# Optimization experiments

Hardware: AMD Instinct MI355X
Metric: run time of the kernel (lower is better)

Reference implementation:

```python
import jax, jax.numpy as jnp
import numpy as np

RADIUS = 1.0      # cfg['radius']
NEAR = 0.5        # cfg['near']
N_STEPS = 32      # cfg['ray_marching_steps']
N_SECANT = 8      # n_secant_steps in unisurf()
TAU = 0.5         # occupancy decision threshold
EPS = 1e-6        # module-level epsilon


def _occ(p, W1, b1, W2, b2):
    # stand-in occupancy network: [..., 3] -> [...]
    h = jax.nn.relu(p @ W1 + b1)
    return jax.nn.sigmoid(h @ W2 + b2)[..., 0]


def get_sphere_intersection(cam_loc, rays, r=RADIUS):
    # cam_loc: [B,3], rays: [B,P,3] (unit). Faithful to the torch version.
    ray_cam_dot = jnp.einsum('bpd,bd->bp', rays, cam_loc)                    # [B,P]
    under_sqrt = ray_cam_dot ** 2 - (jnp.sum(cam_loc ** 2, -1, keepdims=True) - r * r)
    mask_intersect = under_sqrt > 0
    s = jnp.sqrt(jnp.where(mask_intersect, under_sqrt, 0.0))
    inter = jnp.stack([-s - ray_cam_dot, s - ray_cam_dot], axis=-1)          # [B,P,2]
    inter = jnp.where(mask_intersect[..., None], inter, 0.0)
    return jnp.maximum(inter, 0.0), mask_intersect


def setup_inputs() -> dict:
    key = jax.random.key(0)
    k1, k2, k3, k4, k5, k6 = jax.random.split(key, 6)
    B, P, H = 1, 131072, 32
    # camera ~2 units from origin; rays aimed at points near the unit sphere
    cam_loc = jnp.array([[0.0, 0.0, 2.0]], dtype=jnp.float32) + 0.01 * jax.random.normal(k1, (B, 3))
    targets = 0.3 * jax.random.normal(k2, (B, P, 3))
    ray_directions = (targets - cam_loc[:, None, :]).astype(jnp.float32)
    W1 = (0.8 * jax.random.normal(k3, (3, H))).astype(jnp.float32)
    b1 = (0.1 * jax.random.normal(k4, (H,))).astype(jnp.float32)
    W2 = (0.5 * jax.random.normal(k5, (H, 1))).astype(jnp.float32)
    b2 = (0.1 * jax.random.normal(k6, (1,))).astype(jnp.float32)
    return {"cam_loc": cam_loc, "ray_directions": ray_directions,
            "W1": W1, "b1": b1, "W2": W2, "b2": b2}


def reference(cam_loc, ray_directions, W1, b1, W2, b2):
    rays = ray_directions / jnp.linalg.norm(ray_directions, axis=-1, keepdims=True)
    inter, mask_int = get_sphere_intersection(cam_loc, rays, RADIUS)
    far = jnp.maximum(inter[..., 1], NEAR + EPS)                             # [B,P]

    # coarse march: N_STEPS samples per ray between near and sphere-far
    t = jnp.linspace(0.0, 1.0, N_STEPS, dtype=jnp.float32)                   # [S]
    d = NEAR * (1.0 - t) + far[..., None] * t                                # [B,P,S]
    p = cam_loc[:, None, None, :] + rays[:, :, None, :] * d[..., None]       # [B,P,S,3]
    f = _occ(p, W1, b1, W2, b2) - TAU                                        # [B,P,S]

    # first free->occupied sign change (masked-index pattern, vectorized)
    cross = (f[..., :-1] < 0) & (f[..., 1:] >= 0)                            # [B,P,S-1]
    found = jnp.any(cross, axis=-1) & mask_int                               # [B,P]
    idx = jnp.argmax(cross, axis=-1)                                         # [B,P]

    def take(a, i):
        return jnp.take_along_axis(a, i[..., None], axis=-1)[..., 0]

    d_low, f_low = take(d, idx), take(f, idx)
    d_high, f_high = take(d, idx + 1), take(f, idx + 1)

    def secant_body(_, c):
        dl, fl, dh, fh = c
        den = fh - fl
        den = jnp.where(jnp.abs(den) < EPS, EPS, den)
        dm = dl - fl * (dh - dl) / den
        pm = cam_loc[:, None, :] + rays * dm[..., None]
        fm = _occ(pm, W1, b1, W2, b2) - TAU
        neg = fm < 0
        return (jnp.where(neg, dm, dl), jnp.where(neg, fm, fl),
                jnp.where(neg, dh, dm), jnp.where(neg, fh, fm))

    d_low, f_low, d_high, f_high = jax.lax.fori_loop(
        0, N_SECANT, secant_body, (d_low, f_low, d_high, f_high))
    den = f_high - f_low
    den = jnp.where(jnp.abs(den) < EPS, EPS, den)
    d_mid = d_low - f_low * (d_high - d_low) / den
    d_pred = jnp.where(found, d_mid, 0.0)                                    # [B,P]

    # surface points fed back to the model (depth detached, as in torch)
    p_surf = cam_loc[:, None, :] + rays * jax.lax.stop_gradient(d_pred)[..., None]
    occ_surf = jnp.where(found, _occ(p_surf, W1, b1, W2, b2), 0.0)           # [B,P]
    return d_pred, occ_surf
```

## Files before the change

### kernel.cpp

```cpp
#include <hip/hip_runtime.h>
#include <math.h>

#define HDIM 32
#define NSTEPS 32
#define NSECANT 8
#define RADIUSV 1.0f
#define NEARV 0.5f
#define TAUV 0.5f
#define EPSV 1e-6f

typedef float f2 __attribute__((ext_vector_type(2)));

__global__ __launch_bounds__(256) void unisurf_kernel(
    const float* __restrict__ cam_loc,
    const float* __restrict__ ray_dirs,
    const float* __restrict__ W1,
    const float* __restrict__ b1,
    const float* __restrict__ W2,
    const float* __restrict__ b2,
    float* __restrict__ out,
    int P)
{
    __shared__ float4 sW[HDIM];
    __shared__ float  sW2[HDIM];
    __shared__ float  sB2;

    const int tid = threadIdx.x;
    if (tid < HDIM) {
        sW[tid] = make_float4(W1[tid], W1[HDIM + tid], W1[2 * HDIM + tid], b1[tid]);
        sW2[tid] = W2[tid];
    }
    if (tid == 0) sB2 = b2[0];
    __syncthreads();

    const int i = blockIdx.x * blockDim.x + tid;
    if (i >= P) return;

    const float cx = cam_loc[0], cy = cam_loc[1], cz = cam_loc[2];

    float dx = ray_dirs[3 * i + 0];
    float dy = ray_dirs[3 * i + 1];
    float dz = ray_dirs[3 * i + 2];
    float nrm = sqrtf(dx * dx + dy * dy + dz * dz);
    float rx = dx / nrm, ry = dy / nrm, rz = dz / nrm;

    float rcd = rx * cx + ry * cy + rz * cz;
    float c2  = cx * cx + cy * cy + cz * cz;
    float us  = rcd * rcd - (c2 - RADIUSV * RADIUSV);
    bool  mask_int = us > 0.0f;
    float s_sq = mask_int ? sqrtf(us) : 0.0f;
    float far_raw = mask_int ? fmaxf(s_sq - rcd, 0.0f) : 0.0f;
    float farv = fmaxf(far_raw, NEARV + EPSV);

    f2 rW[HDIM / 2], cW[HDIM / 2], w2[HDIM / 2];
    #pragma unroll
    for (int h = 0; h < HDIM / 2; ++h) {
        float4 wa = sW[2 * h], wb = sW[2 * h + 1];
        rW[h] = (f2){rx * wa.x + ry * wa.y + rz * wa.z,
                     rx * wb.x + ry * wb.y + rz * wb.z};
        cW[h] = (f2){cx * wa.x + cy * wa.y + cz * wa.z + wa.w,
                     cx * wb.x + cy * wb.y + cz * wb.z + wb.w};
        w2[h] = (f2){sW2[2 * h], sW2[2 * h + 1]};
    }
    const float B2 = sB2;
    const f2 z2 = (f2){0.0f, 0.0f};

    auto logit = [&](float d) -> float {
        f2 dv = (f2){d, d};
        f2 a0 = z2, a1 = z2, a2 = z2, a3 = z2;
        #pragma unroll
        for (int h = 0; h < HDIM / 2; h += 4) {
            f2 x0 = __builtin_elementwise_fma(dv, rW[h + 0], cW[h + 0]);
            f2 x1 = __builtin_elementwise_fma(dv, rW[h + 1], cW[h + 1]);
            f2 x2 = __builtin_elementwise_fma(dv, rW[h + 2], cW[h + 2]);
            f2 x3 = __builtin_elementwise_fma(dv, rW[h + 3], cW[h + 3]);
            a0 = __builtin_elementwise_fma(__builtin_elementwise_max(x0, z2), w2[h + 0], a0);
            a1 = __builtin_elementwise_fma(__builtin_elementwise_max(x1, z2), w2[h + 1], a1);
            a2 = __builtin_elementwise_fma(__builtin_elementwise_max(x2, z2), w2[h + 2], a2);
            a3 = __builtin_elementwise_fma(__builtin_elementwise_max(x3, z2), w2[h + 3], a3);
        }
        f2 aa = (a0 + a1) + (a2 + a3);
        return (aa.x + aa.y) + B2;
    };
    auto sigm = [](float x) -> float {
        float e = __expf(-x);
        return __builtin_amdgcn_rcpf(1.0f + e);
    };

    float l_prev = logit(NEARV);
    float d_prev = NEARV;
    const float l0 = l_prev;
    float d1v = 0.0f, l1v = 0.0f;

    bool found = false;
    float d_lo = 0.0f, l_lo = 0.0f, d_hi = 0.0f, l_hi = 0.0f;

    const float STEPC = 0.03225806451612903f;
    #pragma unroll 2
    for (int s = 1; s < NSTEPS; ++s) {
        float t = (float)s * STEPC;
        float dd = NEARV * (1.0f - t) + farv * t;
        float ls = logit(dd);
        if (s == 1) { d1v = dd; l1v = ls; }
        if (!found && (l_prev < 0.0f) && (ls >= 0.0f)) {
            found = true;
            d_lo = d_prev; l_lo = l_prev;
            d_hi = dd;     l_hi = ls;
        }
        d_prev = dd; l_prev = ls;
    }
    if (!found) {
        d_lo = NEARV; l_lo = l0;
        d_hi = d1v;   l_hi = l1v;
    }
    found = found && mask_int;

    float f_lo = sigm(l_lo) - TAUV;
    float f_hi = sigm(l_hi) - TAUV;

    #pragma unroll 1
    for (int it = 0; it < NSECANT; ++it) {
        float den = f_hi - f_lo;
        den = (fabsf(den) < EPSV) ? EPSV : den;
        float dm = d_lo - f_lo * (d_hi - d_lo) * __builtin_amdgcn_rcpf(den);
        float fm = sigm(logit(dm)) - TAUV;
        bool neg = fm < 0.0f;
        d_lo = neg ? dm : d_lo;
        f_lo = neg ? fm : f_lo;
        d_hi = neg ? d_hi : dm;
        f_hi = neg ? f_hi : fm;
    }
    float den = f_hi - f_lo;
    den = (fabsf(den) < EPSV) ? EPSV : den;
    float d_mid = d_lo - f_lo * (d_hi - d_lo) * __builtin_amdgcn_rcpf(den);

    float d_pred = found ? d_mid : 0.0f;
    float occ_s = sigm(logit(d_pred));
    float occ_surf = found ? occ_s : 0.0f;

    out[i]     = d_pred;
    out[P + i] = occ_surf;
}

extern "C" void kernel_launch(void* const* d_in, const int* in_sizes, int n_in,
                              void* d_out, int out_size, void* d_ws, size_t ws_size,
                              hipStream_t stream) {
    const float* cam_loc  = (const float*)d_in[0];
    const float* ray_dirs = (const float*)d_in[1];
    const float* W1       = (const float*)d_in[2];
    const float* b1       = (const float*)d_in[3];
    const float* W2       = (const float*)d_in[4];
    const float* b2       = (const float*)d_in[5];
    float* out = (float*)d_out;

    const int P = in_sizes[1] / 3;
    const int block = 256;
    const int grid = (P + block - 1) / block;
    unisurf_kernel<<<grid, block, 0, stream>>>(cam_loc, ray_dirs, W1, b1, W2, b2, out, P);
}
```

Measured before the change: 21.04 us.

## Split each ray's MLP across two lanes and combine with ds_swizzle

Each ray is now handled by a pair of adjacent threads. Each thread evaluates half of the 32 hidden units, and the partial logits are summed through a ds_swizzle pair exchange, so both lanes follow the same marching and secant control flow. This doubles the thread count and halves per-thread registers and FMA work, aiming to raise occupancy and hide latency on a grid that was otherwise small. The cost is duplicated scalar work per ray (normalization, loop control, secant updates) and an extra cross-lane exchange on every network evaluation.

Measured after the change: 22.65 us. 1.08x slower.

```diff
diff --git a/kernel.cpp b/kernel.cpp
--- a/kernel.cpp
+++ b/kernel.cpp
@@ -10,6 +10,11 @@
 #define EPSV 1e-6f
 
 typedef float f2 __attribute__((ext_vector_type(2)));
+
+__device__ __forceinline__ float pair_other(float x) {
+    return __builtin_bit_cast(float,
+        __builtin_amdgcn_ds_swizzle(__builtin_bit_cast(int, x), 0x041F));
+}
 
 __global__ __launch_bounds__(256) void unisurf_kernel(
     const float* __restrict__ cam_loc,
@@ -33,14 +38,17 @@
     if (tid == 0) sB2 = b2[0];
     __syncthreads();
 
-    const int i = blockIdx.x * blockDim.x + tid;
-    if (i >= P) return;
+    const int j = blockIdx.x * blockDim.x + tid;
+    const int r = j >> 1;
+    if (r >= P) return;
+    const int sub = j & 1;
+    const int ubase = sub * (HDIM / 2);
 
     const float cx = cam_loc[0], cy = cam_loc[1], cz = cam_loc[2];
 
-    float dx = ray_dirs[3 * i + 0];
-    float dy = ray_dirs[3 * i + 1];
-    float dz = ray_dirs[3 * i + 2];
+    float dx = ray_dirs[3 * r + 0];
+    float dy = ray_dirs[3 * r + 1];
+    float dz = ray_dirs[3 * r + 2];
     float nrm = sqrtf(dx * dx + dy * dy + dz * dz);
     float rx = dx / nrm, ry = dy / nrm, rz = dz / nrm;
 
@@ -52,15 +60,15 @@
     float far_raw = mask_int ? fmaxf(s_sq - rcd, 0.0f) : 0.0f;
     float farv = fmaxf(far_raw, NEARV + EPSV);
 
-    f2 rW[HDIM / 2], cW[HDIM / 2], w2[HDIM / 2];
+    f2 rW[8], cW[8], w2[8];
     #pragma unroll
-    for (int h = 0; h < HDIM / 2; ++h) {
-        float4 wa = sW[2 * h], wb = sW[2 * h + 1];
-        rW[h] = (f2){rx * wa.x + ry * wa.y + rz * wa.z,
+    for (int k = 0; k < 8; ++k) {
+        float4 wa = sW[ubase + 2 * k], wb = sW[ubase + 2 * k + 1];
+        rW[k] = (f2){rx * wa.x + ry * wa.y + rz * wa.z,
                      rx * wb.x + ry * wb.y + rz * wb.z};
-        cW[h] = (f2){cx * wa.x + cy * wa.y + cz * wa.z + wa.w,
+        cW[k] = (f2){cx * wa.x + cy * wa.y + cz * wa.z + wa.w,
                      cx * wb.x + cy * wb.y + cz * wb.z + wb.w};
-        w2[h] = (f2){sW2[2 * h], sW2[2 * h + 1]};
+        w2[k] = (f2){sW2[ubase + 2 * k], sW2[ubase + 2 * k + 1]};
     }
     const float B2 = sB2;
     const f2 z2 = (f2){0.0f, 0.0f};
@@ -69,18 +77,19 @@
         f2 dv = (f2){d, d};
         f2 a0 = z2, a1 = z2, a2 = z2, a3 = z2;
         #pragma unroll
-        for (int h = 0; h < HDIM / 2; h += 4) {
-            f2 x0 = __builtin_elementwise_fma(dv, rW[h + 0], cW[h + 0]);
-            f2 x1 = __builtin_elementwise_fma(dv, rW[h + 1], cW[h + 1]);
-            f2 x2 = __builtin_elementwise_fma(dv, rW[h + 2], cW[h + 2]);
-            f2 x3 = __builtin_elementwise_fma(dv, rW[h + 3], cW[h + 3]);
-            a0 = __builtin_elementwise_fma(__builtin_elementwise_max(x0, z2), w2[h + 0], a0);
-            a1 = __builtin_elementwise_fma(__builtin_elementwise_max(x1, z2), w2[h + 1], a1);
-            a2 = __builtin_elementwise_fma(__builtin_elementwise_max(x2, z2), w2[h + 2], a2);
-            a3 = __builtin_elementwise_fma(__builtin_elementwise_max(x3, z2), w2[h + 3], a3);
+        for (int k = 0; k < 8; k += 4) {
+            f2 x0 = __builtin_elementwise_fma(dv, rW[k + 0], cW[k + 0]);
+            f2 x1 = __builtin_elementwise_fma(dv, rW[k + 1], cW[k + 1]);
+            f2 x2 = __builtin_elementwise_fma(dv, rW[k + 2], cW[k + 2]);
+            f2 x3 = __builtin_elementwise_fma(dv, rW[k + 3], cW[k + 3]);
+            a0 = __builtin_elementwise_fma(__builtin_elementwise_max(x0, z2), w2[k + 0], a0);
+            a1 = __builtin_elementwise_fma(__builtin_elementwise_max(x1, z2), w2[k + 1], a1);
+            a2 = __builtin_elementwise_fma(__builtin_elementwise_max(x2, z2), w2[k + 2], a2);
+            a3 = __builtin_elementwise_fma(__builtin_elementwise_max(x3, z2), w2[k + 3], a3);
         }
         f2 aa = (a0 + a1) + (a2 + a3);
-        return (aa.x + aa.y) + B2;
+        float p = aa.x + aa.y;
+        return p + pair_other(p) + B2;
     };
     auto sigm = [](float x) -> float {
         float e = __expf(-x);
@@ -138,8 +147,8 @@
     float occ_s = sigm(logit(d_pred));
     float occ_surf = found ? occ_s : 0.0f;
 
-    out[i]     = d_pred;
-    out[P + i] = occ_surf;
+    if (sub == 0) out[r] = d_pred;
+    else          out[P + r] = occ_surf;
 }
 
 extern "C" void kernel_launch(void* const* d_in, const int* in_sizes, int n_in,
@@ -155,6 +164,7 @@
 
     const int P = in_sizes[1] / 3;
     const int block = 256;
-    const int grid = (P + block - 1) / block;
+    const long long total = 2LL * P;
+    const int grid = (int)((total + block - 1) / block);
     unisurf_kernel<<<grid, block, 0, stream>>>(cam_loc, ray_dirs, W1, b1, W2, b2, out, P);
 }
```

## Split each ray's coarse march across two lanes and merge via swizzle

Applied to the files above, without the earlier changes.

Each ray is now handled by a pair of lanes. Each lane evaluates 16 of the 32 coarse samples (even or odd steps) and records the sign of each sample in a bitmask. The two masks are exchanged with ds_swizzle, and the first negative-to-nonnegative crossing is found with ctz. Both lanes then repeat the bracket logits and the secant refinement, and each lane writes one of the two outputs. This doubles the thread count and shortens each thread's serial chain to raise occupancy and latency hiding, at the cost of duplicated secant work and more total ALU operations.

New measurement: 23.98 us. +14.0%, slower.

```diff
diff --git a/kernel.cpp b/kernel.cpp
--- a/kernel.cpp
+++ b/kernel.cpp
@@ -10,6 +10,10 @@
 #define EPSV 1e-6f
 
 typedef float f2 __attribute__((ext_vector_type(2)));
+
+__device__ __forceinline__ unsigned pair_other_u(unsigned x) {
+    return (unsigned)__builtin_amdgcn_ds_swizzle((int)x, 0x041F);
+}
 
 __global__ __launch_bounds__(256) void unisurf_kernel(
     const float* __restrict__ cam_loc,
@@ -33,14 +37,16 @@
     if (tid == 0) sB2 = b2[0];
     __syncthreads();
 
-    const int i = blockIdx.x * blockDim.x + tid;
-    if (i >= P) return;
+    const int j = blockIdx.x * blockDim.x + tid;
+    const int r = j >> 1;
+    if (r >= P) return;
+    const int sub = j & 1;
 
     const float cx = cam_loc[0], cy = cam_loc[1], cz = cam_loc[2];
 
-    float dx = ray_dirs[3 * i + 0];
-    float dy = ray_dirs[3 * i + 1];
-    float dz = ray_dirs[3 * i + 2];
+    float dx = ray_dirs[3 * r + 0];
+    float dy = ray_dirs[3 * r + 1];
+    float dz = ray_dirs[3 * r + 2];
     float nrm = sqrtf(dx * dx + dy * dy + dz * dz);
     float rx = dx / nrm, ry = dy / nrm, rz = dz / nrm;
 
@@ -87,36 +93,36 @@
         return __builtin_amdgcn_rcpf(1.0f + e);
     };
 
-    float l_prev = logit(NEARV);
-    float d_prev = NEARV;
-    const float l0 = l_prev;
-    float d1v = 0.0f, l1v = 0.0f;
+    const float STEPC = 0.03225806451612903f;
 
-    bool found = false;
-    float d_lo = 0.0f, l_lo = 0.0f, d_hi = 0.0f, l_hi = 0.0f;
-
-    const float STEPC = 0.03225806451612903f;
-    #pragma unroll 2
-    for (int s = 1; s < NSTEPS; ++s) {
-        float t = (float)s * STEPC;
+    unsigned msk = 0u;
+    #pragma unroll
+    for (int k = 0; k < 16; ++k) {
+        float t = (float)(sub + 2 * k) * STEPC;
         float dd = NEARV * (1.0f - t) + farv * t;
         float ls = logit(dd);
-        if (s == 1) { d1v = dd; l1v = ls; }
-        if (!found && (l_prev < 0.0f) && (ls >= 0.0f)) {
-            found = true;
-            d_lo = d_prev; l_lo = l_prev;
-            d_hi = dd;     l_hi = ls;
-        }
-        d_prev = dd; l_prev = ls;
+        msk |= (ls >= 0.0f) ? (1u << k) : 0u;
     }
-    if (!found) {
-        d_lo = NEARV; l_lo = l0;
-        d_hi = d1v;   l_hi = l1v;
-    }
+
+    unsigned om = pair_other_u(msk);
+    unsigned E = sub ? om : msk;
+    unsigned O = sub ? msk : om;
+
+    unsigned candE = (~E & O) & 0xFFFFu;
+    unsigned candO = (~O & (E >> 1)) & 0x7FFFu;
+    int sE = candE ? 2 * __builtin_ctz(candE) : 1000;
+    int sO = candO ? 2 * __builtin_ctz(candO) + 1 : 1000;
+    int sstar = sE < sO ? sE : sO;
+    bool found = sstar < 1000;
+    if (!found) sstar = 0;
     found = found && mask_int;
 
-    float f_lo = sigm(l_lo) - TAUV;
-    float f_hi = sigm(l_hi) - TAUV;
+    float tlo = (float)sstar * STEPC;
+    float thi = (float)(sstar + 1) * STEPC;
+    float d_lo = NEARV * (1.0f - tlo) + farv * tlo;
+    float d_hi = NEARV * (1.0f - thi) + farv * thi;
+    float f_lo = sigm(logit(d_lo)) - TAUV;
+    float f_hi = sigm(logit(d_hi)) - TAUV;
 
     #pragma unroll 1
     for (int it = 0; it < NSECANT; ++it) {
@@ -138,8 +144,8 @@
     float occ_s = sigm(logit(d_pred));
     float occ_surf = found ? occ_s : 0.0f;
 
-    out[i]     = d_pred;
-    out[P + i] = occ_surf;
+    if (sub == 0) out[r] = d_pred;
+    else          out[P + r] = occ_surf;
 }
 
 extern "C" void kernel_launch(void* const* d_in, const int* in_sizes, int n_in,
@@ -155,6 +161,7 @@
 
     const int P = in_sizes[1] / 3;
     const int block = 256;
-    const int grid = (P + block - 1) / block;
+    const long long total = 2LL * P;
+    const int grid = (int)((total + block - 1) / block);
     unisurf_kernel<<<grid, block, 0, stream>>>(cam_loc, ray_dirs, W1, b1, W2, b2, out, P);
 }
```
